# Performance work log

Measured on AMD Instinct MI355X. Metric: run time of the kernel, lower is better.

Reference implementation:

```python
import jax, jax.numpy as jnp
import numpy as np

IN_FEATURES, OUT_FEATURES, KERNEL_DIMS = 1024, 128, 8
BATCH = 256


def setup_inputs() -> dict:
    key = jax.random.key(0)
    kx, kT = jax.random.split(key)
    x = jax.random.normal(kx, (BATCH, IN_FEATURES), dtype=jnp.float32)
    T = jax.random.normal(kT, (IN_FEATURES, OUT_FEATURES, KERNEL_DIMS), dtype=jnp.float32)
    return {"x": x, "T": T}


def reference(x, T):
    B = x.shape[0]
    in_f, out_f, kd = T.shape
    # M: (B, out_features, kernel_dims)
    M = (x @ T.reshape(in_f, out_f * kd)).reshape(B, out_f, kd)
    # pairwise L1 distance over kernel dims: (B, B, out_features)
    diffs = jnp.abs(M[None, :, :, :] - M[:, None, :, :]).sum(axis=3)
    # similarity features: sum over other samples, subtract self-term (exp(0)=1)
    c = jnp.exp(-diffs).sum(axis=1) - 1.0  # (B, out_features)
    return jnp.concatenate([x, c], axis=1)
```

## Files before the change

kernel.cpp:

```cpp
#include <hip/hip_runtime.h>
#include <hip/hip_bf16.h>
#include <stdint.h>

#define BATCH 256
#define INF   1024
#define OUTF  128
#define KD    8
#define NN    1024
#define OROW  1152

typedef __attribute__((ext_vector_type(8))) short short8;
typedef __attribute__((ext_vector_type(4))) float f32x4;

__device__ __forceinline__ unsigned short f2bf(float f) {
    union { float f; uint32_t u; } v; v.f = f;
    uint32_t r = v.u + 0x7FFFu + ((v.u >> 16) & 1u);
    return (unsigned short)(r >> 16);
}

__global__ __launch_bounds__(256) void prep_kernel(
    const float* __restrict__ x, const float* __restrict__ T,
    float* __restrict__ out, unsigned short* __restrict__ xbf,
    unsigned short* __restrict__ Tt)
{
    __shared__ unsigned short lds[64 * 65];
    int bid = blockIdx.x;
    int t = threadIdx.x;
    if (bid < 256) {
        int i0 = (bid >> 4) << 6;
        int n0 = (bid & 15) << 6;
        int tx = t & 63, ty = t >> 6;
        for (int r = ty; r < 64; r += 4) {
            float v = T[(size_t)(i0 + r) * NN + n0 + tx];
            lds[tx * 65 + r] = f2bf(v);
        }
        __syncthreads();
        for (int p = 0; p < 8; ++p) {
            int q = p * 512 + t * 2;
            int n = q >> 6, i = q & 63;
            uint32_t u = (uint32_t)lds[n * 65 + i] | ((uint32_t)lds[n * 65 + i + 1] << 16);
            *(uint32_t*)(Tt + (size_t)(n0 + n) * INF + i0 + i) = u;
        }
    } else {
        int bx = bid - 256;
        for (int p = 0; p < 4; ++p) {
            int a = bx * 4 + p;
            int j = t * 4;
            float4 v = *(const float4*)(x + (size_t)a * INF + j);
            *(float4*)(out + (size_t)a * OROW + j) = v;
            uint2 u;
            u.x = (uint32_t)f2bf(v.x) | ((uint32_t)f2bf(v.y) << 16);
            u.y = (uint32_t)f2bf(v.z) | ((uint32_t)f2bf(v.w) << 16);
            *(uint2*)(xbf + (size_t)a * INF + j) = u;
        }
        for (int s = t; s < 512; s += 256) {
            int f = bx * 512 + s;
            int a = f >> 7, o = f & 127;
            out[(size_t)a * OROW + INF + o] = -1.0f;
        }
    }
}

__global__ __launch_bounds__(128) void gemm_kernel(
    const unsigned short* __restrict__ xbf,
    const unsigned short* __restrict__ Tt,
    float* __restrict__ M)
{
    __shared__ float lds[64 * 16];
    int bid = blockIdx.x;
    int a0 = (bid & 7) << 5;
    int n0 = (bid >> 3) << 5;
    int t = threadIdx.x;
    int wave = t >> 6, lane = t & 63;
    int rc = lane & 15, quad = lane >> 4;
    int k0 = wave * 512 + quad * 8;

    f32x4 acc[2][2] = {{{0.f,0.f,0.f,0.f},{0.f,0.f,0.f,0.f}},
                       {{0.f,0.f,0.f,0.f},{0.f,0.f,0.f,0.f}}};
    const unsigned short* pa0 = xbf + (size_t)(a0 + rc) * INF + k0;
    const unsigned short* pa1 = pa0 + 16 * INF;
    const unsigned short* pb0 = Tt + (size_t)(n0 + rc) * INF + k0;
    const unsigned short* pb1 = pb0 + 16 * INF;
#pragma unroll 4
    for (int s = 0; s < 16; ++s) {
        int k = s * 32;
        short8 af0 = *(const short8*)(pa0 + k);
        short8 af1 = *(const short8*)(pa1 + k);
        short8 bg0 = *(const short8*)(pb0 + k);
        short8 bg1 = *(const short8*)(pb1 + k);
        acc[0][0] = __builtin_amdgcn_mfma_f32_16x16x32_bf16(af0, bg0, acc[0][0], 0, 0, 0);
        acc[0][1] = __builtin_amdgcn_mfma_f32_16x16x32_bf16(af0, bg1, acc[0][1], 0, 0, 0);
        acc[1][0] = __builtin_amdgcn_mfma_f32_16x16x32_bf16(af1, bg0, acc[1][0], 0, 0, 0);
        acc[1][1] = __builtin_amdgcn_mfma_f32_16x16x32_bf16(af1, bg1, acc[1][1], 0, 0, 0);
    }
    if (wave == 1) {
        for (int h = 0; h < 2; ++h)
            for (int g = 0; g < 2; ++g)
                for (int r = 0; r < 4; ++r)
                    lds[lane * 16 + (h * 2 + g) * 4 + r] = acc[h][g][r];
    }
    __syncthreads();
    if (wave == 0) {
        for (int h = 0; h < 2; ++h)
            for (int g = 0; g < 2; ++g)
                for (int r = 0; r < 4; ++r) {
                    float v = acc[h][g][r] + lds[lane * 16 + (h * 2 + g) * 4 + r];
                    int rr = a0 + h * 16 + quad * 4 + r;
                    int cc = n0 + g * 16 + rc;
                    M[(size_t)rr * NN + cc] = v;
                }
    }
}

__global__ __launch_bounds__(256) void pair_kernel(
    const float* __restrict__ M, float* __restrict__ out)
{
    int o = blockIdx.x >> 1;
    int half = blockIdx.x & 1;
    int a = threadIdx.x;
    const float* ma = M + (size_t)a * NN + o * KD;
    float4 m0 = *(const float4*)(ma);
    float4 m1 = *(const float4*)(ma + 4);
    float ssum = 0.f;
    int b0 = half * 128;
#pragma unroll 4
    for (int b = b0; b < b0 + 128; ++b) {
        const float* mb = M + (size_t)b * NN + o * KD;
        float4 q0 = *(const float4*)(mb);
        float4 q1 = *(const float4*)(mb + 4);
        float d = fabsf(m0.x - q0.x) + fabsf(m0.y - q0.y)
                + fabsf(m0.z - q0.z) + fabsf(m0.w - q0.w)
                + fabsf(m1.x - q1.x) + fabsf(m1.y - q1.y)
                + fabsf(m1.z - q1.z) + fabsf(m1.w - q1.w);
        ssum += __expf(-d);
    }
    atomicAdd(out + (size_t)a * OROW + INF + o, ssum);
}

extern "C" void kernel_launch(void* const* d_in, const int* in_sizes, int n_in,
                              void* d_out, int out_size, void* d_ws, size_t ws_size,
                              hipStream_t stream) {
    const float* x = (const float*)d_in[0];
    const float* T = (const float*)d_in[1];
    float* out = (float*)d_out;
    unsigned short* xbf = (unsigned short*)d_ws;
    unsigned short* Tt  = (unsigned short*)((char*)d_ws + 524288);
    float*          M   = (float*)((char*)d_ws + 524288 + 2097152);

    prep_kernel<<<320, 256, 0, stream>>>(x, T, out, xbf, Tt);
    gemm_kernel<<<256, 128, 0, stream>>>(xbf, Tt, M);
    pair_kernel<<<256, 256, 0, stream>>>(M, out);
}
```

Baseline: 81.90 us.

## Fuse prep, GEMM and pairwise stages into one kernel per output feature

Replaces three launches (convert/transpose, GEMM, pairwise) with a single kernel where each block owns one output feature. The block gathers and converts its T slice into LDS and computes the 256x8 M slice with MFMA, converting x to bf16 on the fly. It then does the pairwise exp-sum from LDS and writes the result directly, with no atomics and no M round trip through global memory. This removes launch overheads and intermediate global traffic. The cost is that x is reread and reconverted by all 128 blocks, T reads are strided gathers, and only 128 compute blocks run.

New measurement: 96.78 us. 18.2% more time.

```diff
diff --git a/kernel.cpp b/kernel.cpp
--- a/kernel.cpp
+++ b/kernel.cpp
@@ -6,126 +6,100 @@
 #define INF   1024
 #define OUTF  128
 #define KD    8
-#define NN    1024
 #define OROW  1152
+
+#define TSLS 1032
+#define MLS  12
 
 typedef __attribute__((ext_vector_type(8))) short short8;
 typedef __attribute__((ext_vector_type(4))) float f32x4;
 
 __device__ __forceinline__ unsigned short f2bf(float f) {
-    union { float f; uint32_t u; } v; v.f = f;
-    uint32_t r = v.u + 0x7FFFu + ((v.u >> 16) & 1u);
-    return (unsigned short)(r >> 16);
+    __hip_bfloat16 h = __float2bfloat16(f);
+    union { __hip_bfloat16 h; unsigned short u; } v; v.h = h;
+    return v.u;
 }
 
-__global__ __launch_bounds__(256) void prep_kernel(
+__global__ __launch_bounds__(512) void fused_kernel(
     const float* __restrict__ x, const float* __restrict__ T,
-    float* __restrict__ out, unsigned short* __restrict__ xbf,
-    unsigned short* __restrict__ Tt)
+    float* __restrict__ out)
 {
-    __shared__ unsigned short lds[64 * 65];
-    int bid = blockIdx.x;
-    int t = threadIdx.x;
-    if (bid < 256) {
-        int i0 = (bid >> 4) << 6;
-        int n0 = (bid & 15) << 6;
-        int tx = t & 63, ty = t >> 6;
-        for (int r = ty; r < 64; r += 4) {
-            float v = T[(size_t)(i0 + r) * NN + n0 + tx];
-            lds[tx * 65 + r] = f2bf(v);
+    const int bid = blockIdx.x;
+    const int t = threadIdx.x;
+
+    if (bid >= OUTF) {
+        const int bx = bid - OUTF;
+        const float4* xs = (const float4*)x;
+        #pragma unroll
+        for (int p = 0; p < 2; ++p) {
+            int g = bx * 1024 + p * 512 + t;
+            int row = g >> 8, col4 = g & 255;
+            float4 v = xs[g];
+            *(float4*)(out + (size_t)row * OROW + col4 * 4) = v;
         }
-        __syncthreads();
-        for (int p = 0; p < 8; ++p) {
-            int q = p * 512 + t * 2;
-            int n = q >> 6, i = q & 63;
-            uint32_t u = (uint32_t)lds[n * 65 + i] | ((uint32_t)lds[n * 65 + i + 1] << 16);
-            *(uint32_t*)(Tt + (size_t)(n0 + n) * INF + i0 + i) = u;
-        }
-    } else {
-        int bx = bid - 256;
-        for (int p = 0; p < 4; ++p) {
-            int a = bx * 4 + p;
-            int j = t * 4;
-            float4 v = *(const float4*)(x + (size_t)a * INF + j);
-            *(float4*)(out + (size_t)a * OROW + j) = v;
-            uint2 u;
-            u.x = (uint32_t)f2bf(v.x) | ((uint32_t)f2bf(v.y) << 16);
-            u.y = (uint32_t)f2bf(v.z) | ((uint32_t)f2bf(v.w) << 16);
-            *(uint2*)(xbf + (size_t)a * INF + j) = u;
-        }
-        for (int s = t; s < 512; s += 256) {
-            int f = bx * 512 + s;
-            int a = f >> 7, o = f & 127;
-            out[(size_t)a * OROW + INF + o] = -1.0f;
+        return;
+    }
+
+    __shared__ __align__(16) unsigned short Tsl[8 * TSLS];
+    __shared__ __align__(16) float Mloc[256 * MLS];
+    __shared__ float red[256];
+
+    const int o = bid;
+
+    for (int i = t; i < 8192; i += 512) {
+        int kd = i & 7, k = i >> 3;
+        Tsl[kd * TSLS + k] = f2bf(T[(size_t)k * (OUTF * KD) + o * KD + kd]);
+    }
+    __syncthreads();
+
+    const int wave = t >> 6, lane = t & 63;
+    const int rc = lane & 15, quad = lane >> 4;
+    const int abase = wave * 32;
+
+    f32x4 acc0 = {0.f, 0.f, 0.f, 0.f}, acc1 = {0.f, 0.f, 0.f, 0.f};
+    const float* pa0 = x + (size_t)(abase + rc) * INF + quad * 8;
+    const float* pa1 = pa0 + 16 * INF;
+    const unsigned short* pb = Tsl + (rc & 7) * TSLS + quad * 8;
+
+    #pragma unroll 4
+    for (int ks = 0; ks < 32; ++ks) {
+        const int k = ks * 32;
+        float4 a0l = *(const float4*)(pa0 + k);
+        float4 a0h = *(const float4*)(pa0 + k + 4);
+        float4 a1l = *(const float4*)(pa1 + k);
+        float4 a1h = *(const float4*)(pa1 + k + 4);
+        short8 bf = *(const short8*)(pb + k);
+        short8 a0f, a1f;
+        a0f[0] = (short)f2bf(a0l.x); a0f[1] = (short)f2bf(a0l.y);
+        a0f[2] = (short)f2bf(a0l.z); a0f[3] = (short)f2bf(a0l.w);
+        a0f[4] = (short)f2bf(a0h.x); a0f[5] = (short)f2bf(a0h.y);
+        a0f[6] = (short)f2bf(a0h.z); a0f[7] = (short)f2bf(a0h.w);
+        a1f[0] = (short)f2bf(a1l.x); a1f[1] = (short)f2bf(a1l.y);
+        a1f[2] = (short)f2bf(a1l.z); a1f[3] = (short)f2bf(a1l.w);
+        a1f[4] = (short)f2bf(a1h.x); a1f[5] = (short)f2bf(a1h.y);
+        a1f[6] = (short)f2bf(a1h.z); a1f[7] = (short)f2bf(a1h.w);
+        acc0 = __builtin_amdgcn_mfma_f32_16x16x32_bf16(a0f, bf, acc0, 0, 0, 0);
+        acc1 = __builtin_amdgcn_mfma_f32_16x16x32_bf16(a1f, bf, acc1, 0, 0, 0);
+    }
+
+    if (rc < 8) {
+        #pragma unroll
+        for (int r = 0; r < 4; ++r) {
+            Mloc[(abase + quad * 4 + r) * MLS + rc]      = acc0[r];
+            Mloc[(abase + 16 + quad * 4 + r) * MLS + rc] = acc1[r];
         }
     }
-}
+    __syncthreads();
 
-__global__ __launch_bounds__(128) void gemm_kernel(
-    const unsigned short* __restrict__ xbf,
-    const unsigned short* __restrict__ Tt,
-    float* __restrict__ M)
-{
-    __shared__ float lds[64 * 16];
-    int bid = blockIdx.x;
-    int a0 = (bid & 7) << 5;
-    int n0 = (bid >> 3) << 5;
-    int t = threadIdx.x;
-    int wave = t >> 6, lane = t & 63;
-    int rc = lane & 15, quad = lane >> 4;
-    int k0 = wave * 512 + quad * 8;
-
-    f32x4 acc[2][2] = {{{0.f,0.f,0.f,0.f},{0.f,0.f,0.f,0.f}},
-                       {{0.f,0.f,0.f,0.f},{0.f,0.f,0.f,0.f}}};
-    const unsigned short* pa0 = xbf + (size_t)(a0 + rc) * INF + k0;
-    const unsigned short* pa1 = pa0 + 16 * INF;
-    const unsigned short* pb0 = Tt + (size_t)(n0 + rc) * INF + k0;
-    const unsigned short* pb1 = pb0 + 16 * INF;
-#pragma unroll 4
-    for (int s = 0; s < 16; ++s) {
-        int k = s * 32;
-        short8 af0 = *(const short8*)(pa0 + k);
-        short8 af1 = *(const short8*)(pa1 + k);
-        short8 bg0 = *(const short8*)(pb0 + k);
-        short8 bg1 = *(const short8*)(pb1 + k);
-        acc[0][0] = __builtin_amdgcn_mfma_f32_16x16x32_bf16(af0, bg0, acc[0][0], 0, 0, 0);
-        acc[0][1] = __builtin_amdgcn_mfma_f32_16x16x32_bf16(af0, bg1, acc[0][1], 0, 0, 0);
-        acc[1][0] = __builtin_amdgcn_mfma_f32_16x16x32_bf16(af1, bg0, acc[1][0], 0, 0, 0);
-        acc[1][1] = __builtin_amdgcn_mfma_f32_16x16x32_bf16(af1, bg1, acc[1][1], 0, 0, 0);
-    }
-    if (wave == 1) {
-        for (int h = 0; h < 2; ++h)
-            for (int g = 0; g < 2; ++g)
-                for (int r = 0; r < 4; ++r)
-                    lds[lane * 16 + (h * 2 + g) * 4 + r] = acc[h][g][r];
-    }
-    __syncthreads();
-    if (wave == 0) {
-        for (int h = 0; h < 2; ++h)
-            for (int g = 0; g < 2; ++g)
-                for (int r = 0; r < 4; ++r) {
-                    float v = acc[h][g][r] + lds[lane * 16 + (h * 2 + g) * 4 + r];
-                    int rr = a0 + h * 16 + quad * 4 + r;
-                    int cc = n0 + g * 16 + rc;
-                    M[(size_t)rr * NN + cc] = v;
-                }
-    }
-}
-
-__global__ __launch_bounds__(256) void pair_kernel(
-    const float* __restrict__ M, float* __restrict__ out)
-{
-    int o = blockIdx.x >> 1;
-    int half = blockIdx.x & 1;
-    int a = threadIdx.x;
-    const float* ma = M + (size_t)a * NN + o * KD;
+    const int a  = t & 255;
+    const int bh = t >> 8;
+    const float* ma = Mloc + a * MLS;
     float4 m0 = *(const float4*)(ma);
     float4 m1 = *(const float4*)(ma + 4);
     float ssum = 0.f;
-    int b0 = half * 128;
-#pragma unroll 4
-    for (int b = b0; b < b0 + 128; ++b) {
-        const float* mb = M + (size_t)b * NN + o * KD;
+    #pragma unroll 4
+    for (int j = 0; j < 128; ++j) {
+        const float* mb = Mloc + (bh * 128 + j) * MLS;
         float4 q0 = *(const float4*)(mb);
         float4 q1 = *(const float4*)(mb + 4);
         float d = fabsf(m0.x - q0.x) + fabsf(m0.y - q0.y)
@@ -134,7 +108,9 @@
                 + fabsf(m1.z - q1.z) + fabsf(m1.w - q1.w);
         ssum += __expf(-d);
     }
-    atomicAdd(out + (size_t)a * OROW + INF + o, ssum);
+    if (bh) red[a] = ssum;
+    __syncthreads();
+    if (!bh) out[(size_t)a * OROW + INF + o] = ssum + red[a] - 1.0f;
 }
 
 extern "C" void kernel_launch(void* const* d_in, const int* in_sizes, int n_in,
@@ -143,11 +119,6 @@
     const float* x = (const float*)d_in[0];
     const float* T = (const float*)d_in[1];
     float* out = (float*)d_out;
-    unsigned short* xbf = (unsigned short*)d_ws;
-    unsigned short* Tt  = (unsigned short*)((char*)d_ws + 524288);
-    float*          M   = (float*)((char*)d_ws + 524288 + 2097152);
-
-    prep_kernel<<<320, 256, 0, stream>>>(x, T, out, xbf, Tt);
-    gemm_kernel<<<256, 128, 0, stream>>>(xbf, Tt, M);
-    pair_kernel<<<256, 256, 0, stream>>>(M, out);
+    (void)d_ws; (void)ws_size;
+    fused_kernel<<<OUTF + 64, 512, 0, stream>>>(x, T, out);
 }
```

## Fuse GEMM and pairwise-similarity kernels with LDS-pipelined x staging

Applied to the files above, without the earlier changes.

Merges the GEMM and pairwise kernels into one kernel per output feature (and batch half). Each block computes the full 256x8 M slice in LDS, using async global_load_lds with a 4-deep ring buffer for x chunks and an XOR-swizzled layout. It then evaluates pairwise exp-L1 sums from LDS and reduces them without atomics. This removes the M round-trip through global memory, one launch, and the -1 init pass. The cost is that each block recomputes the GEMM for all 256 rows, so x is read 256 times and the same work is done twice across the two halves.

New measurement: 70.82 us. -13.5%, faster.

```diff
diff --git a/kernel.cpp b/kernel.cpp
--- a/kernel.cpp
+++ b/kernel.cpp
@@ -1,5 +1,4 @@
 #include <hip/hip_runtime.h>
-#include <hip/hip_bf16.h>
 #include <stdint.h>
 
 #define BATCH 256
@@ -8,6 +7,11 @@
 #define KD    8
 #define NN    1024
 #define OROW  1152
+
+#define TSLP  1040
+#define MLS   12
+#define CHSH  16384
+#define NBUF  4
 
 typedef __attribute__((ext_vector_type(8))) short short8;
 typedef __attribute__((ext_vector_type(4))) float f32x4;
@@ -35,6 +39,7 @@
             lds[tx * 65 + r] = f2bf(v);
         }
         __syncthreads();
+        #pragma unroll
         for (int p = 0; p < 8; ++p) {
             int q = p * 512 + t * 2;
             int n = q >> 6, i = q & 63;
@@ -43,6 +48,7 @@
         }
     } else {
         int bx = bid - 256;
+        #pragma unroll
         for (int p = 0; p < 4; ++p) {
             int a = bx * 4 + p;
             int j = t * 4;
@@ -53,88 +59,132 @@
             u.y = (uint32_t)f2bf(v.z) | ((uint32_t)f2bf(v.w) << 16);
             *(uint2*)(xbf + (size_t)a * INF + j) = u;
         }
-        for (int s = t; s < 512; s += 256) {
-            int f = bx * 512 + s;
-            int a = f >> 7, o = f & 127;
-            out[(size_t)a * OROW + INF + o] = -1.0f;
-        }
-    }
-}
-
-__global__ __launch_bounds__(128) void gemm_kernel(
-    const unsigned short* __restrict__ xbf,
-    const unsigned short* __restrict__ Tt,
-    float* __restrict__ M)
+    }
+}
+
+__device__ __forceinline__ void stage_xb(
+    const unsigned short* __restrict__ xbf, unsigned short* lbuf,
+    int c, int wave, int lane)
 {
-    __shared__ float lds[64 * 16];
-    int bid = blockIdx.x;
-    int a0 = (bid & 7) << 5;
-    int n0 = (bid >> 3) << 5;
-    int t = threadIdx.x;
-    int wave = t >> 6, lane = t & 63;
-    int rc = lane & 15, quad = lane >> 4;
-    int k0 = wave * 512 + quad * 8;
-
-    f32x4 acc[2][2] = {{{0.f,0.f,0.f,0.f},{0.f,0.f,0.f,0.f}},
-                       {{0.f,0.f,0.f,0.f},{0.f,0.f,0.f,0.f}}};
-    const unsigned short* pa0 = xbf + (size_t)(a0 + rc) * INF + k0;
-    const unsigned short* pa1 = pa0 + 16 * INF;
-    const unsigned short* pb0 = Tt + (size_t)(n0 + rc) * INF + k0;
-    const unsigned short* pb1 = pb0 + 16 * INF;
-#pragma unroll 4
-    for (int s = 0; s < 16; ++s) {
-        int k = s * 32;
-        short8 af0 = *(const short8*)(pa0 + k);
-        short8 af1 = *(const short8*)(pa1 + k);
-        short8 bg0 = *(const short8*)(pb0 + k);
-        short8 bg1 = *(const short8*)(pb1 + k);
-        acc[0][0] = __builtin_amdgcn_mfma_f32_16x16x32_bf16(af0, bg0, acc[0][0], 0, 0, 0);
-        acc[0][1] = __builtin_amdgcn_mfma_f32_16x16x32_bf16(af0, bg1, acc[0][1], 0, 0, 0);
-        acc[1][0] = __builtin_amdgcn_mfma_f32_16x16x32_bf16(af1, bg0, acc[1][0], 0, 0, 0);
-        acc[1][1] = __builtin_amdgcn_mfma_f32_16x16x32_bf16(af1, bg1, acc[1][1], 0, 0, 0);
-    }
-    if (wave == 1) {
-        for (int h = 0; h < 2; ++h)
-            for (int g = 0; g < 2; ++g)
-                for (int r = 0; r < 4; ++r)
-                    lds[lane * 16 + (h * 2 + g) * 4 + r] = acc[h][g][r];
-    }
+    const int rin = lane >> 3;
+    const int seg = lane & 7;
+    #pragma unroll
+    for (int p = 0; p < 4; ++p) {
+        const int i = wave * 4 + p;
+        const unsigned short* src = xbf + (size_t)(i * 8 + rin) * INF
+                                        + c * 64 + ((seg ^ rin) << 3);
+        unsigned short* dst = lbuf + i * 512;
+        __builtin_amdgcn_global_load_lds(
+            (const __attribute__((address_space(1))) unsigned int*)src,
+            (__attribute__((address_space(3))) unsigned int*)dst, 16, 0, 0);
+    }
+}
+
+#define GEMM_STEP(c, VM) do {                                                 \
+    const uint32_t bb = xlsBase + (uint32_t)(((c) & 3) << 15);                \
+    const uint32_t tb = tslBase + (uint32_t)((c) << 7);                       \
+    short8 A00, A01, A10, A11, B0, B1;                                        \
+    asm volatile(                                                             \
+        "s_waitcnt vmcnt(" #VM ")\n\t"                                        \
+        "ds_read_b128 %0, %6\n\t"                                             \
+        "ds_read_b128 %1, %7\n\t"                                             \
+        "ds_read_b128 %2, %8\n\t"                                             \
+        "ds_read_b128 %3, %9\n\t"                                             \
+        "ds_read_b128 %4, %10\n\t"                                            \
+        "ds_read_b128 %5, %11\n\t"                                            \
+        "s_waitcnt lgkmcnt(0)"                                                \
+        : "=v"(A00), "=v"(A01), "=v"(A10), "=v"(A11), "=v"(B0), "=v"(B1)      \
+        : "v"(bb + oA00), "v"(bb + oA01), "v"(bb + oA10), "v"(bb + oA11),     \
+          "v"(tb + oB0), "v"(tb + oB1)                                        \
+        : "memory");                                                          \
+    acc0 = __builtin_amdgcn_mfma_f32_16x16x32_bf16(A00, B0, acc0, 0, 0, 0);   \
+    acc0 = __builtin_amdgcn_mfma_f32_16x16x32_bf16(A01, B1, acc0, 0, 0, 0);   \
+    acc1 = __builtin_amdgcn_mfma_f32_16x16x32_bf16(A10, B0, acc1, 0, 0, 0);   \
+    acc1 = __builtin_amdgcn_mfma_f32_16x16x32_bf16(A11, B1, acc1, 0, 0, 0);   \
+} while (0)
+
+__global__ __launch_bounds__(512, 1) void fused_kernel(
+    const unsigned short* __restrict__ xbf, const unsigned short* __restrict__ Tt,
+    float* __restrict__ out)
+{
+    __shared__ __align__(16) unsigned short xls[NBUF * CHSH];
+    __shared__ __align__(16) union {
+        unsigned short Tsl[KD * TSLP];
+        float red[512];
+    } u;
+    __shared__ __align__(16) float Mloc[256 * MLS];
+
+    const int o = blockIdx.x >> 1;
+    const int half = blockIdx.x & 1;
+    const int t = threadIdx.x;
+    const int wave = t >> 6, lane = t & 63;
+
+    #pragma unroll
+    for (int p = 0; p < 2; ++p) {
+        const unsigned short* src = Tt + (size_t)(o * 8 + wave) * INF + p * 512 + lane * 8;
+        unsigned short* dst = u.Tsl + wave * TSLP + p * 512;
+        __builtin_amdgcn_global_load_lds(
+            (const __attribute__((address_space(1))) unsigned int*)src,
+            (__attribute__((address_space(3))) unsigned int*)dst, 16, 0, 0);
+    }
+    stage_xb(xbf, xls + 0 * CHSH, 0, wave, lane);
+    stage_xb(xbf, xls + 1 * CHSH, 1, wave, lane);
+    stage_xb(xbf, xls + 2 * CHSH, 2, wave, lane);
     __syncthreads();
-    if (wave == 0) {
-        for (int h = 0; h < 2; ++h)
-            for (int g = 0; g < 2; ++g)
-                for (int r = 0; r < 4; ++r) {
-                    float v = acc[h][g][r] + lds[lane * 16 + (h * 2 + g) * 4 + r];
-                    int rr = a0 + h * 16 + quad * 4 + r;
-                    int cc = n0 + g * 16 + rc;
-                    M[(size_t)rr * NN + cc] = v;
-                }
-    }
-}
-
-__global__ __launch_bounds__(256) void pair_kernel(
-    const float* __restrict__ M, float* __restrict__ out)
-{
-    int o = blockIdx.x >> 1;
-    int half = blockIdx.x & 1;
-    int a = threadIdx.x;
-    const float* ma = M + (size_t)a * NN + o * KD;
-    float4 m0 = *(const float4*)(ma);
-    float4 m1 = *(const float4*)(ma + 4);
+
+    const int rc = lane & 15, quad = lane >> 4, r7 = rc & 7;
+    const int abase = wave * 32;
+    f32x4 acc0 = {0.f, 0.f, 0.f, 0.f}, acc1 = {0.f, 0.f, 0.f, 0.f};
+
+    const uint32_t xlsBase = (uint32_t)(uintptr_t)(&xls[0]);
+    const uint32_t tslBase = (uint32_t)(uintptr_t)(&u.Tsl[0]);
+    const uint32_t rowA = (uint32_t)((abase + rc) * 128);
+    const uint32_t oA00 = rowA + (uint32_t)(((0 * 4 + quad) ^ r7) << 4);
+    const uint32_t oA01 = rowA + (uint32_t)(((1 * 4 + quad) ^ r7) << 4);
+    const uint32_t oA10 = oA00 + 2048, oA11 = oA01 + 2048;
+    const uint32_t oB0 = (uint32_t)(r7 * 2080 + quad * 16);
+    const uint32_t oB1 = oB0 + 64;
+
+    for (int c = 0; c < 13; ++c) {
+        stage_xb(xbf, xls + ((c + 3) & 3) * CHSH, c + 3, wave, lane);
+        GEMM_STEP(c, 12);
+    }
+    GEMM_STEP(13, 8);
+    GEMM_STEP(14, 4);
+    GEMM_STEP(15, 0);
+
+    if (rc < 8) {
+        #pragma unroll
+        for (int r = 0; r < 4; ++r) {
+            Mloc[(abase + quad * 4 + r) * MLS + rc]      = acc0[r];
+            Mloc[(abase + 16 + quad * 4 + r) * MLS + rc] = acc1[r];
+        }
+    }
+    __syncthreads();
+
+    const int ar = t & 127;
+    const int bq = t >> 7;
+    const int a = half * 128 + ar;
+    f32x4 m0 = *(const f32x4*)(Mloc + a * MLS);
+    f32x4 m1 = *(const f32x4*)(Mloc + a * MLS + 4);
     float ssum = 0.f;
-    int b0 = half * 128;
-#pragma unroll 4
-    for (int b = b0; b < b0 + 128; ++b) {
-        const float* mb = M + (size_t)b * NN + o * KD;
-        float4 q0 = *(const float4*)(mb);
-        float4 q1 = *(const float4*)(mb + 4);
-        float d = fabsf(m0.x - q0.x) + fabsf(m0.y - q0.y)
-                + fabsf(m0.z - q0.z) + fabsf(m0.w - q0.w)
-                + fabsf(m1.x - q1.x) + fabsf(m1.y - q1.y)
-                + fabsf(m1.z - q1.z) + fabsf(m1.w - q1.w);
+    #pragma unroll 4
+    for (int j = 0; j < 64; ++j) {
+        const float* qp = Mloc + (bq * 64 + j) * MLS;
+        f32x4 q0 = *(const f32x4*)(qp);
+        f32x4 q1 = *(const f32x4*)(qp + 4);
+        float d = fabsf(m0[0] - q0[0]) + fabsf(m0[1] - q0[1])
+                + fabsf(m0[2] - q0[2]) + fabsf(m0[3] - q0[3])
+                + fabsf(m1[0] - q1[0]) + fabsf(m1[1] - q1[1])
+                + fabsf(m1[2] - q1[2]) + fabsf(m1[3] - q1[3]);
         ssum += __expf(-d);
     }
-    atomicAdd(out + (size_t)a * OROW + INF + o, ssum);
+    u.red[t] = ssum;
+    __syncthreads();
+    if (t < 128) {
+        float s = u.red[t] + u.red[t + 128] + u.red[t + 256] + u.red[t + 384];
+        out[(size_t)(half * 128 + t) * OROW + INF + o] = s - 1.0f;
+    }
 }
 
 extern "C" void kernel_launch(void* const* d_in, const int* in_sizes, int n_in,
@@ -145,9 +195,7 @@
     float* out = (float*)d_out;
     unsigned short* xbf = (unsigned short*)d_ws;
     unsigned short* Tt  = (unsigned short*)((char*)d_ws + 524288);
-    float*          M   = (float*)((char*)d_ws + 524288 + 2097152);
 
     prep_kernel<<<320, 256, 0, stream>>>(x, T, out, xbf, Tt);
-    gemm_kernel<<<256, 128, 0, stream>>>(xbf, Tt, M);
-    pair_kernel<<<256, 256, 0, stream>>>(M, out);
-}
+    fused_kernel<<<256, 512, 0, stream>>>(xbf, Tt, out);
+}
```
